# Kernel optimization log

Hardware: AMD Instinct MI355X
Metric: run time of the kernel (lower is better)

## Reference

```python
import jax, jax.numpy as jnp
import numpy as np

BATCH, SEQ, IN_DIM, UNITS = 32, 512, 512, 1024


def setup_inputs() -> dict:
    key = jax.random.key(0)
    k1, k2, k3 = jax.random.split(key, 3)
    data = jax.random.normal(k1, (BATCH, SEQ, IN_DIM), dtype=jnp.float32)
    Wx = jax.random.normal(k2, (IN_DIM, 4 * UNITS), dtype=jnp.float32) * 0.02
    Wh = jax.random.normal(k3, (UNITS, 4 * UNITS), dtype=jnp.float32) * 0.02
    b = jnp.zeros((4 * UNITS,), dtype=jnp.float32)
    return {"data": data, "Wx": Wx, "Wh": Wh, "b": b}


def reference(data, Wx, Wh, b):
    # Precompute input projections for all timesteps at once: [B, T, 4U]
    x_proj = jnp.einsum("bti,iu->btu", data, Wx) + b
    units = Wh.shape[0]
    B = data.shape[0]

    def step(carry, xp_t):
        h, c = carry
        gates = xp_t + h @ Wh  # [B, 4U]
        i, f, g, o = jnp.split(gates, 4, axis=-1)
        i = jax.nn.sigmoid(i)
        f = jax.nn.sigmoid(f)
        g = jnp.tanh(g)
        o = jax.nn.sigmoid(o)
        c_new = f * c + i * g
        h_new = o * jnp.tanh(c_new)
        return (h_new, c_new), h_new

    h0 = jnp.zeros((B, units), dtype=data.dtype)
    c0 = jnp.zeros((B, units), dtype=data.dtype)
    # scan over time axis: xs is [T, B, 4U]
    (_, _), hs = jax.lax.scan(step, (h0, c0), jnp.swapaxes(x_proj, 0, 1))
    # return_sequences=True -> [B, T, U]
    return jnp.swapaxes(hs, 0, 1)
```

## Files before the change

### kernel.cpp

```cpp
#include <hip/hip_runtime.h>
#include <cstdint>
#include <cstddef>

typedef __bf16 bf16x8 __attribute__((ext_vector_type(8)));
typedef __bf16 bf16x4 __attribute__((ext_vector_type(4)));
typedef float  f32x4  __attribute__((ext_vector_type(4)));

#define WS_WFRAG   0
#define WS_XB      12582912
#define WS_XCHG    29360128
#define WS_CNT     62914560
#define WS_NEEDED  62930944

#define LDS_BYTES  163840

__device__ __forceinline__ void gload16(const void* g, void* l) {
    __builtin_amdgcn_global_load_lds(
        (const __attribute__((address_space(1))) void*)(g),
        (__attribute__((address_space(3))) void*)(l),
        16, 0, 0);
}

__device__ __forceinline__ float sigmoidf_(float x) {
    return 1.f / (1.f + __expf(-x));
}
__device__ __forceinline__ float tanhf_(float x) {
    x = fminf(fmaxf(x, -15.f), 15.f);
    float e2 = __expf(2.f * x);
    return (e2 - 1.f) / (e2 + 1.f);
}

__global__ void __launch_bounds__(256) prep_w_kernel(const float* __restrict__ Wx,
                                                     const float* __restrict__ Wh,
                                                     __bf16* __restrict__ wfrag) {
    int tid = blockIdx.x * 256 + threadIdx.x;
    int l   = tid & 63;
    int m   = tid >> 6;
    int nt  = m & 1;
    int sk  = m >> 1;
    int kk  = sk % 48;
    int s   = sk / 48;
    int lc  = l & 15;
    int c   = nt * 16 + lc;
    int uu  = c >> 2;
    int gi  = c & 3;
    int n   = gi * 1024 + s * 8 + uu;
    int k0  = kk * 32 + (l >> 4) * 8;
    bf16x8 v;
#pragma unroll
    for (int j = 0; j < 8; ++j) {
        int k  = k0 + j;
        float f = (k < 512) ? Wx[k * 4096 + n] : Wh[(k - 512) * 4096 + n];
        v[j] = (__bf16)f;
    }
    ((bf16x8*)wfrag)[tid] = v;
}

__global__ void __launch_bounds__(256) prep_x_kernel(const float* __restrict__ data,
                                                     __bf16* __restrict__ xb) {
    int tid = blockIdx.x * 256 + threadIdx.x;
    float4 v = ((const float4*)data)[tid];
    bf16x4 o;
    o[0] = (__bf16)v.x; o[1] = (__bf16)v.y; o[2] = (__bf16)v.z; o[3] = (__bf16)v.w;
    ((bf16x4*)xb)[tid] = o;
}

__global__ void __launch_bounds__(128)
lstm_main(const __bf16* __restrict__ xb, const __bf16* __restrict__ wfrag,
          const float* __restrict__ bias, float* __restrict__ out,
          __bf16* __restrict__ hbuf, unsigned* __restrict__ cnt) {
    extern __shared__ char smem[];
    __bf16* X_lds = (__bf16*)smem;
    __bf16* H_lds = (__bf16*)(smem + 32768);
    __bf16* W_lds = (__bf16*)(smem + 65536);

    const int tid = threadIdx.x;
    const int l   = tid & 63;
    const int w   = tid >> 6;
    const int q   = l >> 4;
    const int r   = l & 15;
    const int bid = blockIdx.x;
    const int s   = bid & 127;
    const int g   = bid >> 7;
    const int gb0 = g * 16;

    const __bf16* wsrc = wfrag + (size_t)s * 49152;
    for (int m = w * 48; m < w * 48 + 48; ++m) {
        gload16(wsrc + m * 512 + l * 8, W_lds + m * 512);
    }

    const int uu = w * 4 + q;
    const int u  = s * 8 + uu;
    const float b_i = bias[u];
    const float b_f = bias[1024 + u];
    const float b_g = bias[2048 + u];
    const float b_o = bias[3072 + u];
    float cst = 0.f;

    unsigned* cbase = cnt + g * 1024;
    unsigned* mycnt = cbase + (s & 15) * 64;
    unsigned* flag  = cnt + 2048 + g * 64;

    {
        const __bf16* xrow = xb + (size_t)(gb0 + r) * 512 * 512;
#pragma unroll
        for (int j = 0; j < 8; ++j) {
            int m = w * 8 + j;
            gload16(xrow + m * 32 + q * 8, X_lds + m * 512);
        }
    }

    __syncthreads();

    for (int t = 0; t < 512; ++t) {
        unsigned long long va[16], vb[16];
        {
            const __bf16* hsrc = hbuf + (size_t)t * 32768 + (size_t)g * 16384;
#pragma unroll
            for (int j = 0; j < 16; ++j) {
                int m = w * 16 + j;
                ulonglong2 v = *(const ulonglong2*)(hsrc + (m * 4 + q) * 128 + r * 8);
                va[j] = v.x; vb[j] = v.y;
            }
        }

        const __bf16* Xc = X_lds + (t & 1) * 8192;
        f32x4 acc0 = {0.f, 0.f, 0.f, 0.f};
        f32x4 acc1 = {0.f, 0.f, 0.f, 0.f};
#pragma unroll
        for (int kk = 0; kk < 16; kk += 2) {
            bf16x8 a0 = *(const bf16x8*)(Xc + kk * 512 + l * 8);
            bf16x8 b0 = *(const bf16x8*)(W_lds + (kk * 2 + w) * 512 + l * 8);
            acc0 = __builtin_amdgcn_mfma_f32_16x16x32_bf16(a0, b0, acc0, 0, 0, 0);
            bf16x8 a1 = *(const bf16x8*)(Xc + (kk + 1) * 512 + l * 8);
            bf16x8 b1 = *(const bf16x8*)(W_lds + ((kk + 1) * 2 + w) * 512 + l * 8);
            acc1 = __builtin_amdgcn_mfma_f32_16x16x32_bf16(a1, b1, acc1, 0, 0, 0);
        }

#pragma unroll
        for (int j = 0; j < 16; ++j) {
            int m = w * 16 + j;
            unsigned long long tmp[2] = {va[j], vb[j]};
            *((ulonglong2*)(H_lds + m * 512 + l * 8)) = *(const ulonglong2*)tmp;
        }
        __syncthreads();

#pragma unroll 4
        for (int kk = 16; kk < 48; kk += 2) {
            bf16x8 a0 = *(const bf16x8*)(H_lds + (kk - 16) * 512 + l * 8);
            bf16x8 b0 = *(const bf16x8*)(W_lds + (kk * 2 + w) * 512 + l * 8);
            acc0 = __builtin_amdgcn_mfma_f32_16x16x32_bf16(a0, b0, acc0, 0, 0, 0);
            bf16x8 a1 = *(const bf16x8*)(H_lds + (kk - 15) * 512 + l * 8);
            bf16x8 b1 = *(const bf16x8*)(W_lds + ((kk + 1) * 2 + w) * 512 + l * 8);
            acc1 = __builtin_amdgcn_mfma_f32_16x16x32_bf16(a1, b1, acc1, 0, 0, 0);
        }

        float*  scr   = (float*)(smem + ((t + 1) & 1) * 16384);
        __bf16* hpack = (__bf16*)(smem + ((t + 1) & 1) * 16384 + 2176);
        float* sw = scr + w * 272;
#pragma unroll
        for (int rg = 0; rg < 4; ++rg) {
            sw[(l & 15) * 17 + q * 4 + rg] = acc0[rg] + acc1[rg];
        }
        float xi = sw[(q * 4 + 0) * 17 + r];
        float xf = sw[(q * 4 + 1) * 17 + r];
        float xg = sw[(q * 4 + 2) * 17 + r];
        float xo = sw[(q * 4 + 3) * 17 + r];

        float ii = sigmoidf_(xi + b_i);
        float ff = sigmoidf_(xf + b_f);
        float gg = tanhf_(xg + b_g);
        float oo = sigmoidf_(xo + b_o);
        cst = ff * cst + ii * gg;
        float h = oo * tanhf_(cst);

        const int bglob = gb0 + r;

        if (t < 511) {
            hpack[r * 8 + uu] = (__bf16)h;
            __syncthreads();
            if (w == 0) {
                if (tid < 32) {
                    unsigned long long v = ((const unsigned long long*)hpack)[tid];
                    unsigned long long* dst = (unsigned long long*)
                        (hbuf + (size_t)(t + 1) * 32768 + (size_t)g * 16384 + s * 128) + tid;
                    __hip_atomic_store(dst, v, __ATOMIC_RELAXED, __HIP_MEMORY_SCOPE_AGENT);
                }
                __asm__ __volatile__("s_waitcnt vmcnt(0)" ::: "memory");
                if (tid == 0) {
                    __hip_atomic_fetch_add(mycnt, 1u, __ATOMIC_RELAXED, __HIP_MEMORY_SCOPE_AGENT);
                }
            }
            out[((size_t)bglob * 512 + t) * 1024 + u] = h;
            {
                const __bf16* xrow = xb + ((size_t)(gb0 + r) * 512 + (t + 1)) * 512;
                __bf16* Xn = X_lds + ((t + 1) & 1) * 8192;
#pragma unroll
                for (int j = 0; j < 8; ++j) {
                    int m = w * 8 + j;
                    gload16(xrow + m * 32 + q * 8, Xn + m * 512);
                }
            }
            if (tid == 0) {
                if (s == 0) {
                    const unsigned target = 128u * (unsigned)(t + 1);
                    for (;;) {
                        unsigned sum = 0;
#pragma unroll
                        for (int i = 0; i < 16; ++i)
                            sum += __hip_atomic_load(cbase + i * 64, __ATOMIC_RELAXED,
                                                     __HIP_MEMORY_SCOPE_AGENT);
                        if (sum >= target) break;
                    }
                    __hip_atomic_store(flag, (unsigned)(t + 1), __ATOMIC_RELAXED,
                                       __HIP_MEMORY_SCOPE_AGENT);
                } else {
                    while (__hip_atomic_load(flag, __ATOMIC_RELAXED,
                                             __HIP_MEMORY_SCOPE_AGENT) < (unsigned)(t + 1)) {}
                }
            }
            __syncthreads();
        } else {
            out[((size_t)bglob * 512 + t) * 1024 + u] = h;
        }
    }
}

extern "C" void kernel_launch(void* const* d_in, const int* in_sizes, int n_in,
                              void* d_out, int out_size, void* d_ws, size_t ws_size,
                              hipStream_t stream) {
    const float* data = (const float*)d_in[0];
    const float* Wx   = (const float*)d_in[1];
    const float* Wh   = (const float*)d_in[2];
    const float* b    = (const float*)d_in[3];
    float* out = (float*)d_out;

    if (ws_size < (size_t)WS_NEEDED) return;

    char* ws = (char*)d_ws;
    __bf16*   wfrag = (__bf16*)(ws + WS_WFRAG);
    __bf16*   xbuf  = (__bf16*)(ws + WS_XB);
    __bf16*   xchg  = (__bf16*)(ws + WS_XCHG);
    unsigned* cnt   = (unsigned*)(ws + WS_CNT);

    hipFuncSetAttribute((const void*)lstm_main,
                        hipFuncAttributeMaxDynamicSharedMemorySize, LDS_BYTES);

    prep_w_kernel<<<3072, 256, 0, stream>>>(Wx, Wh, wfrag);
    prep_x_kernel<<<8192, 256, 0, stream>>>(data, xbuf);
    hipMemsetAsync(ws + WS_XCHG, 0x00, 65536, stream);
    hipMemsetAsync(ws + WS_CNT,  0x00, 16384, stream);

    lstm_main<<<256, 128, LDS_BYTES, stream>>>(xbuf, wfrag, b, out, xchg, cnt);
}
```

Baseline: 1.844 ms.

## Replace centralized grid barrier with per-block flags and sentinel-polled h exchange

```diff
diff --git a/kernel.cpp b/kernel.cpp
--- a/kernel.cpp
+++ b/kernel.cpp
@@ -13,6 +13,8 @@
 #define WS_NEEDED  62930944
 
 #define LDS_BYTES  163840
+
+#define SENT 0xFFFFFFFFFFFFFFFFULL
 
 __device__ __forceinline__ void gload16(const void* g, void* l) {
     __builtin_amdgcn_global_load_lds(
@@ -97,9 +99,7 @@
     const float b_o = bias[3072 + u];
     float cst = 0.f;
 
-    unsigned* cbase = cnt + g * 1024;
-    unsigned* mycnt = cbase + (s & 15) * 64;
-    unsigned* flag  = cnt + 2048 + g * 64;
+    unsigned* fl = cnt + g * 1024;
 
     {
         const __bf16* xrow = xb + (size_t)(gb0 + r) * 512 * 512;
@@ -113,15 +113,19 @@
     __syncthreads();
 
     for (int t = 0; t < 512; ++t) {
+        if (t > 0) {
+            const unsigned tgt = (unsigned)t;
+            while (__hip_atomic_load(fl + w * 64 + l, __ATOMIC_RELAXED,
+                                     __HIP_MEMORY_SCOPE_AGENT) < tgt) {}
+        }
+
         unsigned long long va[16], vb[16];
-        {
-            const __bf16* hsrc = hbuf + (size_t)t * 32768 + (size_t)g * 16384;
-#pragma unroll
-            for (int j = 0; j < 16; ++j) {
-                int m = w * 16 + j;
-                ulonglong2 v = *(const ulonglong2*)(hsrc + (m * 4 + q) * 128 + r * 8);
-                va[j] = v.x; vb[j] = v.y;
-            }
+        const __bf16* hsrc = hbuf + (size_t)t * 32768 + (size_t)g * 16384;
+#pragma unroll
+        for (int j = 0; j < 16; ++j) {
+            int m = w * 16 + j;
+            ulonglong2 v = *(const ulonglong2*)(hsrc + (m * 4 + q) * 128 + r * 8);
+            va[j] = v.x; vb[j] = v.y;
         }
 
         const __bf16* Xc = X_lds + (t & 1) * 8192;
@@ -135,6 +139,27 @@
             bf16x8 a1 = *(const bf16x8*)(Xc + (kk + 1) * 512 + l * 8);
             bf16x8 b1 = *(const bf16x8*)(W_lds + ((kk + 1) * 2 + w) * 512 + l * 8);
             acc1 = __builtin_amdgcn_mfma_f32_16x16x32_bf16(a1, b1, acc1, 0, 0, 0);
+        }
+
+        if (t > 0) {
+            for (;;) {
+                int miss = 0;
+#pragma unroll
+                for (int j = 0; j < 16; ++j)
+                    miss += (va[j] == SENT) + (vb[j] == SENT);
+                if (miss == 0) break;
+                __builtin_amdgcn_s_sleep(1);
+#pragma unroll
+                for (int j = 0; j < 16; ++j) {
+                    int m = w * 16 + j;
+                    const unsigned long long* p =
+                        (const unsigned long long*)(hsrc + (m * 4 + q) * 128 + r * 8);
+                    if (va[j] == SENT)
+                        va[j] = __hip_atomic_load(p,     __ATOMIC_RELAXED, __HIP_MEMORY_SCOPE_AGENT);
+                    if (vb[j] == SENT)
+                        vb[j] = __hip_atomic_load(p + 1, __ATOMIC_RELAXED, __HIP_MEMORY_SCOPE_AGENT);
+                }
+            }
         }
 
 #pragma unroll
@@ -186,9 +211,9 @@
                         (hbuf + (size_t)(t + 1) * 32768 + (size_t)g * 16384 + s * 128) + tid;
                     __hip_atomic_store(dst, v, __ATOMIC_RELAXED, __HIP_MEMORY_SCOPE_AGENT);
                 }
-                __asm__ __volatile__("s_waitcnt vmcnt(0)" ::: "memory");
                 if (tid == 0) {
-                    __hip_atomic_fetch_add(mycnt, 1u, __ATOMIC_RELAXED, __HIP_MEMORY_SCOPE_AGENT);
+                    __hip_atomic_store(fl + s, (unsigned)(t + 1), __ATOMIC_RELAXED,
+                                       __HIP_MEMORY_SCOPE_AGENT);
                 }
             }
             out[((size_t)bglob * 512 + t) * 1024 + u] = h;
@@ -201,25 +226,6 @@
                     gload16(xrow + m * 32 + q * 8, Xn + m * 512);
                 }
             }
-            if (tid == 0) {
-                if (s == 0) {
-                    const unsigned target = 128u * (unsigned)(t + 1);
-                    for (;;) {
-                        unsigned sum = 0;
-#pragma unroll
-                        for (int i = 0; i < 16; ++i)
-                            sum += __hip_atomic_load(cbase + i * 64, __ATOMIC_RELAXED,
-                                                     __HIP_MEMORY_SCOPE_AGENT);
-                        if (sum >= target) break;
-                    }
-                    __hip_atomic_store(flag, (unsigned)(t + 1), __ATOMIC_RELAXED,
-                                       __HIP_MEMORY_SCOPE_AGENT);
-                } else {
-                    while (__hip_atomic_load(flag, __ATOMIC_RELAXED,
-                                             __HIP_MEMORY_SCOPE_AGENT) < (unsigned)(t + 1)) {}
-                }
-            }
-            __syncthreads();
         } else {
             out[((size_t)bglob * 512 + t) * 1024 + u] = h;
         }
@@ -249,6 +255,7 @@
     prep_w_kernel<<<3072, 256, 0, stream>>>(Wx, Wh, wfrag);
     prep_x_kernel<<<8192, 256, 0, stream>>>(data, xbuf);
     hipMemsetAsync(ws + WS_XCHG, 0x00, 65536, stream);
+    hipMemsetAsync(ws + WS_XCHG + 65536, 0xFF, 33554432 - 65536, stream);
     hipMemsetAsync(ws + WS_CNT,  0x00, 16384, stream);
 
     lstm_main<<<256, 128, LDS_BYTES, stream>>>(xbuf, wfrag, b, out, xchg, cnt);
```

Measured after the change: 2.055 ms. +11.4%, slower.
